# Optimization experiments

Hardware: AMD Instinct MI355X
Metric: run time of the kernel (lower is better)

The kernel has to match this reference:

```python
import jax, jax.numpy as jnp
import numpy as np

HIDDEN = 4096
NUM_HEADS = 32
HEAD_DIM = HIDDEN // NUM_HEADS
B, S = 2, 2048
ROPE_BASE = 10000.0


def setup_inputs() -> dict:
    key = jax.random.key(0)
    k1, k2, k3, k4 = jax.random.split(key, 4)
    hidden_states = jax.random.normal(k1, (B, S, HIDDEN), dtype=jnp.float32)
    positions = jnp.tile(jnp.arange(S, dtype=jnp.int32)[None, :], (B, 1))
    W_qkv = jax.random.normal(k2, (HIDDEN, 3 * HIDDEN), dtype=jnp.float32) * (HIDDEN ** -0.5)
    b_qkv = jax.random.normal(k3, (3 * HIDDEN,), dtype=jnp.float32) * 0.02
    W_o = jax.random.normal(k4, (HIDDEN, HIDDEN), dtype=jnp.float32) * (HIDDEN ** -0.5)
    return {"hidden_states": hidden_states, "positions": positions,
            "W_qkv": W_qkv, "b_qkv": b_qkv, "W_o": W_o}


def _rope(x, positions):
    # x: [B, S, H, D]; GPT-NeoX style full-dim rotary (rotary_dim = head_dim)
    half = HEAD_DIM // 2
    inv_freq = 1.0 / (ROPE_BASE ** (jnp.arange(0, half, dtype=jnp.float32) * 2.0 / HEAD_DIM))
    ang = positions.astype(jnp.float32)[:, :, None] * inv_freq[None, None, :]  # [B,S,half]
    cos = jnp.cos(ang)[:, :, None, :]  # [B,S,1,half]
    sin = jnp.sin(ang)[:, :, None, :]
    x1, x2 = x[..., :half], x[..., half:]
    return jnp.concatenate([x1 * cos - x2 * sin, x2 * cos + x1 * sin], axis=-1)


def reference(hidden_states, positions, W_qkv, b_qkv, W_o):
    qkv = jnp.einsum('bsh,hk->bsk', hidden_states, W_qkv) + b_qkv
    q, k, v = jnp.split(qkv, 3, axis=-1)
    q = q.reshape(B, S, NUM_HEADS, HEAD_DIM)
    k = k.reshape(B, S, NUM_HEADS, HEAD_DIM)
    v = v.reshape(B, S, NUM_HEADS, HEAD_DIM)
    q = _rope(q, positions)
    k = _rope(k, positions)
    scale = HEAD_DIM ** -0.5
    scores = jnp.einsum('bqhd,bkhd->bhqk', q, k) * scale  # [B,H,S,S]
    causal = jnp.tril(jnp.ones((S, S), dtype=bool))
    scores = jnp.where(causal[None, None], scores, jnp.float32(-1e30))
    probs = jax.nn.softmax(scores, axis=-1)
    ctx = jnp.einsum('bhqk,bkhd->bqhd', probs, v).reshape(B, S, HIDDEN)
    return jnp.einsum('bsh,ho->bso', ctx, W_o)
```

## Files before the change

### kernel.cpp

```cpp
#include <hip/hip_runtime.h>
#include <stdint.h>

#define HID 4096
#define NHD 32
#define HD  128
#define BB  2
#define SS  2048
#define BSZ (BB*SS)
#define N3  (3*HID)

typedef __bf16 bf16x8 __attribute__((ext_vector_type(8)));
typedef __bf16 bf16x4 __attribute__((ext_vector_type(4)));
typedef float  f32x4  __attribute__((ext_vector_type(4)));

#define MFMA16(A,B,C) __builtin_amdgcn_mfma_f32_16x16x32_bf16((A),(B),(C),0,0,0)

__device__ __forceinline__ void gl_lds16(const __bf16* g, __bf16* l) {
  __builtin_amdgcn_global_load_lds(
      (__attribute__((address_space(1))) void*)g,
      (__attribute__((address_space(3))) void*)l, 16, 0, 0);
}

__device__ __forceinline__ void block_bar() {
  __builtin_amdgcn_sched_barrier(0);
  __builtin_amdgcn_s_barrier();
  __builtin_amdgcn_sched_barrier(0);
}
#define LGKM0() do { asm volatile("s_waitcnt lgkmcnt(0)" ::: "memory"); \
                     __builtin_amdgcn_sched_barrier(0); } while (0)
#define VMC(n)  do { asm volatile("s_waitcnt vmcnt(" #n ")" ::: "memory"); \
                     __builtin_amdgcn_sched_barrier(0); } while (0)

__global__ void cvt_bf16(const float* __restrict__ in, __bf16* __restrict__ out, int n) {
  int i = (blockIdx.x * blockDim.x + threadIdx.x) * 4;
  if (i >= n) return;
  float4 v = *(const float4*)(in + i);
  bf16x4 r;
  r[0] = (__bf16)v.x; r[1] = (__bf16)v.y; r[2] = (__bf16)v.z; r[3] = (__bf16)v.w;
  *(bf16x4*)(out + i) = r;
}

__global__ void transp_cvt(const float* __restrict__ in, __bf16* __restrict__ out,
                           int R, int C) {
  __shared__ float t[64 * 65];
  int c0 = blockIdx.x * 64, r0 = blockIdx.y * 64;
  int tx = threadIdx.x & 15, ty = threadIdx.x >> 4;
  for (int j = 0; j < 4; ++j) {
    float4 v = *(const float4*)(in + (size_t)(r0 + ty + 16 * j) * C + c0 + tx * 4);
    float* d = t + (ty + 16 * j) * 65 + tx * 4;
    d[0] = v.x; d[1] = v.y; d[2] = v.z; d[3] = v.w;
  }
  __syncthreads();
  for (int j = 0; j < 4; ++j) {
    int cc = ty + 16 * j;
    bf16x4 o4;
    for (int e = 0; e < 4; ++e) o4[e] = (__bf16)t[(tx * 4 + e) * 65 + cc];
    *(bf16x4*)(out + (size_t)(c0 + cc) * R + r0 + tx * 4) = o4;
  }
}


__device__ __forceinline__ void ld_a4(bf16x8 a[4][2], const __bf16* base, int row, int quad) {
#pragma unroll
  for (int m = 0; m < 4; ++m) {
    const int rr = row + m * 16;
    const int sw = rr & 7;
#pragma unroll
    for (int kk = 0; kk < 2; ++kk)
      a[m][kk] = *(const bf16x8*)(base + rr * 64 + ((kk * 4 + quad) ^ sw) * 8);
  }
}
__device__ __forceinline__ void ld_b2(bf16x8 b[2][2], const __bf16* base, int row, int quad) {
#pragma unroll
  for (int n = 0; n < 2; ++n) {
    const int rr = row + n * 16;
    const int sw = rr & 7;
#pragma unroll
    for (int kk = 0; kk < 2; ++kk)
      b[n][kk] = *(const bf16x8*)(base + rr * 64 + ((kk * 4 + quad) ^ sw) * 8);
  }
}
__device__ __forceinline__ void mma_quad(f32x4 acc[8][4], bf16x8 a[4][2],
                                         bf16x8 b[2][2], int mh, int nh) {
  __builtin_amdgcn_s_setprio(1);
#pragma unroll
  for (int m = 0; m < 4; ++m)
#pragma unroll
    for (int n = 0; n < 2; ++n) {
      f32x4 c = acc[mh * 4 + m][nh * 2 + n];
      c = MFMA16(a[m][0], b[n][0], c);
      c = MFMA16(a[m][1], b[n][1], c);
      acc[mh * 4 + m][nh * 2 + n] = c;
    }
  __builtin_amdgcn_s_setprio(0);
}

__device__ __forceinline__ void core256(const __bf16* __restrict__ Ab,
                                        const __bf16* __restrict__ Bb,
                                        int K, __bf16* smem, f32x4 acc[8][4]) {
  const int tid  = threadIdx.x;
  const int wave = tid >> 6, lane = tid & 63;
  const int quad = lane >> 4, l15 = lane & 15;
  const int arow = ((wave >> 2) * 64) + l15;
  const int brow = ((wave & 3) * 32) + l15;
  const int NKT = K >> 6, NIT = NKT >> 1;

  __bf16* aBuf[2] = { smem,          smem + 16384 };
  __bf16* bBuf[2] = { smem + 32768,  smem + 49152 };

  const int off0 = tid * 16, off1 = off0 + 8192;
  const int r0 = off0 >> 7, r1 = off1 >> 7;
  const int sO0 = r0 * K + ((((off0 >> 4) & 7) ^ (r0 & 7)) * 8);
  const int sO1 = r1 * K + ((((off1 >> 4) & 7) ^ (r1 & 7)) * 8);
  const int d0 = off0 >> 1, d1 = off1 >> 1;

#define STG_A(buf, half, kt) do { \
    const __bf16* s_ = Ab + (size_t)(half) * 128 * K + (size_t)(kt) * 64; \
    gl_lds16(s_ + sO0, aBuf[buf] + (half) * 8192 + d0); \
    gl_lds16(s_ + sO1, aBuf[buf] + (half) * 8192 + d1); } while (0)
#define STG_B(buf, half, kt) do { \
    const __bf16* s_ = Bb + (size_t)(half) * 128 * K + (size_t)(kt) * 64; \
    gl_lds16(s_ + sO0, bBuf[buf] + (half) * 8192 + d0); \
    gl_lds16(s_ + sO1, bBuf[buf] + (half) * 8192 + d1); } while (0)

  bf16x8 a_r[4][2], bn0[2][2], bn1[2][2];

  STG_A(0, 0, 0); STG_B(0, 0, 0); STG_B(0, 1, 0); STG_A(0, 1, 0);
  STG_A(1, 0, 1); STG_B(1, 0, 1); STG_B(1, 1, 1);
  VMC(6);
  block_bar();

  for (int i = 0; i < NIT; ++i) {
    const bool last = (i == NIT - 1);
    const int t1 = 2 * i + 1, t2 = 2 * i + 2, t3 = 2 * i + 3;

    ld_a4(a_r, aBuf[0],        arow, quad);
    ld_b2(bn0, bBuf[0],        brow, quad);
    STG_A(1, 1, t1);
    block_bar(); LGKM0();
    mma_quad(acc, a_r, bn0, 0, 0);
    block_bar();

    ld_b2(bn1, bBuf[0] + 8192, brow, quad);
    if (!last) STG_A(0, 0, t2);
    block_bar(); LGKM0();
    mma_quad(acc, a_r, bn1, 0, 1);
    block_bar();

    ld_a4(a_r, aBuf[0] + 8192, arow, quad);
    if (!last) STG_B(0, 0, t2);
    block_bar(); LGKM0();
    mma_quad(acc, a_r, bn1, 1, 1);
    block_bar();

    if (!last) STG_B(0, 1, t2);
    block_bar();
    mma_quad(acc, a_r, bn0, 1, 0);
    if (last) { VMC(0); } else { VMC(6); }
    block_bar();

    ld_a4(a_r, aBuf[1],        arow, quad);
    ld_b2(bn0, bBuf[1],        brow, quad);
    if (!last) STG_A(0, 1, t2);
    block_bar(); LGKM0();
    mma_quad(acc, a_r, bn0, 0, 0);
    block_bar();

    ld_b2(bn1, bBuf[1] + 8192, brow, quad);
    if (!last) STG_A(1, 0, t3);
    block_bar(); LGKM0();
    mma_quad(acc, a_r, bn1, 0, 1);
    block_bar();

    ld_a4(a_r, aBuf[1] + 8192, arow, quad);
    if (!last) STG_B(1, 0, t3);
    block_bar(); LGKM0();
    mma_quad(acc, a_r, bn1, 1, 1);
    block_bar();

    if (!last) STG_B(1, 1, t3);
    block_bar();
    mma_quad(acc, a_r, bn0, 1, 0);
    VMC(6);
    block_bar();
  }
#undef STG_A
#undef STG_B
}

__device__ __forceinline__ int eswz(int r, int c) {
  return r * 256 + ((((c >> 3) ^ (r & 31) ^ (r >> 5)) & 31) * 8) + (c & 7);
}

__global__ __launch_bounds__(512, 2) void gemm_qkv(
    const __bf16* __restrict__ A, const __bf16* __restrict__ Bt,
    const float* __restrict__ bias, const int* __restrict__ pos,
    __bf16* __restrict__ qr, __bf16* __restrict__ kr, __bf16* __restrict__ vt,
    int M, int N, int K) {
  __shared__ __bf16 smem[65536];
  const int tid = threadIdx.x;
  const int wave = tid >> 6, lane = tid & 63;
  const int quad = lane >> 4, l15 = lane & 15;
  const int wm = (wave >> 2) * 64, wn = (wave & 3) * 32;

  const int orig = blockIdx.x;
  const int swz = (orig & 7) * 96 + (orig >> 3);
  const int m0 = (swz & 15) * 256;
  const int n0 = (swz >> 4) * 256;

  f32x4 acc[8][4];
#pragma unroll
  for (int i = 0; i < 8; ++i)
#pragma unroll
    for (int j = 0; j < 4; ++j) acc[i][j] = (f32x4){0.f, 0.f, 0.f, 0.f};

  core256(A + (size_t)m0 * K, Bt + (size_t)n0 * K, K, smem, acc);

#pragma unroll
  for (int ni = 0; ni < 4; ++ni) {
    const int scol = (ni >> 1) * 128 + wn + (ni & 1) * 16 + l15;
    const float bv = bias[n0 + scol];
#pragma unroll
    for (int mi = 0; mi < 8; ++mi) {
      const int rbase = (mi >> 2) * 128 + wm + (mi & 3) * 16 + quad * 4;
#pragma unroll
      for (int rr = 0; rr < 4; ++rr)
        smem[eswz(rbase + rr, scol)] = (__bf16)(acc[mi][ni][rr] + bv);
    }
  }
  __syncthreads();

  const int reg = n0 >> 12;
  const int h0  = (n0 & 4095) >> 7;
  const int b   = m0 >> 11;
  const int s0  = m0 & 2047;

  if (reg == 2) {
    __bf16* dst = vt + (size_t)(b * NHD + h0) * HD * SS;
    const int sg = tid & 31, cb = tid >> 5;
    for (int p = 0; p < 16; ++p) {
      const int c = cb + 16 * p;
      bf16x8 v8;
#pragma unroll
      for (int e = 0; e < 8; ++e) v8[e] = smem[eswz(sg * 8 + e, c)];
      *(bf16x8*)(dst + (size_t)(c >> 7) * HD * SS + (size_t)(c & 127) * SS +
                 s0 + sg * 8) = v8;
    }
  } else {
    __bf16* dst = (reg == 0 ? qr : kr) + (size_t)(b * NHD + h0) * SS * HD;
    const float osc = (reg == 0) ? 0.08838834764831845f : 1.0f;
    const int d2 = tid & 63, rb = (tid >> 6) * 32;
    const float freq = expf(-0.14391156831212787f * (float)d2);
    for (int i = 0; i < 32; ++i) {
      const int r = rb + i;
      const float p = (float)pos[b * SS + s0 + r];
      float sn, cs;
      sincosf(p * freq, &sn, &cs);
#pragma unroll
      for (int hs = 0; hs < 2; ++hs) {
        const float x1 = (float)smem[eswz(r, hs * 128 + d2)];
        const float x2 = (float)smem[eswz(r, hs * 128 + d2 + 64)];
        __bf16* dr = dst + (size_t)hs * SS * HD + (size_t)(s0 + r) * HD;
        dr[d2]      = (__bf16)((x1 * cs - x2 * sn) * osc);
        dr[d2 + 64] = (__bf16)((x2 * cs + x1 * sn) * osc);
      }
    }
  }
}

__global__ __launch_bounds__(512, 2) void gemm_bt(
    const __bf16* __restrict__ A, const __bf16* __restrict__ Bt,
    float* __restrict__ Cout, int M, int N, int K) {
  __shared__ __bf16 smem[65536];
  const int tid = threadIdx.x;
  const int wave = tid >> 6, lane = tid & 63;
  const int quad = lane >> 4, l15 = lane & 15;
  const int wm = (wave >> 2) * 64, wn = (wave & 3) * 32;

  const int orig = blockIdx.x;
  const int swz = (orig & 7) * 32 + (orig >> 3);
  const int m0 = (swz & 15) * 256;
  const int n0 = (swz >> 4) * 256;

  f32x4 acc[8][4];
#pragma unroll
  for (int i = 0; i < 8; ++i)
#pragma unroll
    for (int j = 0; j < 4; ++j) acc[i][j] = (f32x4){0.f, 0.f, 0.f, 0.f};

  core256(A + (size_t)m0 * K, Bt + (size_t)n0 * K, K, smem, acc);

#pragma unroll
  for (int mi = 0; mi < 8; ++mi) {
    const int row = m0 + (mi >> 2) * 128 + wm + (mi & 3) * 16 + quad * 4;
#pragma unroll
    for (int ni = 0; ni < 4; ++ni) {
      const int col = n0 + (ni >> 1) * 128 + wn + (ni & 1) * 16 + l15;
#pragma unroll
      for (int rr = 0; rr < 4; ++rr)
        Cout[(size_t)(row + rr) * N + col] = acc[mi][ni][rr];
    }
  }
}

__global__ __launch_bounds__(256, 2) void flash_attn(
    const __bf16* __restrict__ qr, const __bf16* __restrict__ kr,
    const __bf16* __restrict__ vt, __bf16* __restrict__ ctx) {
  __shared__ __bf16 sK[2][64 * 128];
  __shared__ __bf16 sV[128 * 64];
  __shared__ __bf16 sP[4][32 * 64];
  const int bh = blockIdx.x;
  const int qt = 15 - blockIdx.y;
  const int b = bh >> 5, h = bh & 31;
  const int tid = threadIdx.x;
  const int wave = tid >> 6, lane = tid & 63;
  const int quad = lane >> 4, l15 = lane & 15;
  const int q0 = qt * 128;
  const int NT = 2 * qt + 2;

  const __bf16* qbase = qr + (size_t)bh * SS * HD;
  const __bf16* kbase = kr + (size_t)bh * SS * HD;
  const __bf16* vbase = vt + (size_t)bh * HD * SS;
  __bf16* pw = &sP[wave][0];

#define STG_K(buf_, kt_) do {                                         \
    const __bf16* kb_ = kbase + (size_t)(kt_) * 64 * HD;              \
    _Pragma("unroll")                                                 \
    for (int i_ = 0; i_ < 4; ++i_) {                                  \
      int off_ = tid * 16 + i_ * 4096;                                \
      int r_ = off_ >> 8, cl_ = (off_ >> 4) & 15;                     \
      int cg_ = (cl_ & 8) | ((cl_ & 7) ^ (r_ & 7));                   \
      gl_lds16(kb_ + (size_t)r_ * HD + cg_ * 8, &sK[buf_][0] + (off_ >> 1)); \
    } } while (0)
#define STG_V(kt_) do {                                               \
    const __bf16* vb_ = vbase + (size_t)(kt_) * 64;                   \
    _Pragma("unroll")                                                 \
    for (int i_ = 0; i_ < 4; ++i_) {                                  \
      int off_ = tid * 16 + i_ * 4096;                                \
      int r_ = off_ >> 7, cl_ = (off_ >> 4) & 7;                      \
      int cg_ = cl_ ^ (r_ & 7);                                       \
      gl_lds16(vb_ + (size_t)r_ * SS + cg_ * 8, &sV[0] + (off_ >> 1)); \
    } } while (0)

  bf16x8 qf[2][4];
  for (int im = 0; im < 2; ++im) {
    int row = q0 + wave * 32 + im * 16 + l15;
    for (int ks = 0; ks < 4; ++ks)
      qf[im][ks] = *(const bf16x8*)(qbase + (size_t)row * HD + ks * 32 + quad * 8);
  }

  f32x4 o[2][8];
  for (int im = 0; im < 2; ++im)
    for (int jd = 0; jd < 8; ++jd)
      o[im][jd] = (f32x4){0.f, 0.f, 0.f, 0.f};
  float l_i[2][4];
  for (int im = 0; im < 2; ++im)
    for (int rg = 0; rg < 4; ++rg) l_i[im][rg] = 0.f;

  STG_K(0, 0);

  for (int kt = 0; kt < NT; ++kt) {
    const int k0 = kt * 64;
    const bool more = (kt + 1 < NT);

    block_bar();
    STG_V(kt);
    if (more) STG_K((kt + 1) & 1, kt + 1);
    if (more) { VMC(8); } else { VMC(4); }
    block_bar();

    const __bf16* sKc = &sK[kt & 1][0];

    f32x4 s[2][4];
    for (int im = 0; im < 2; ++im)
      for (int jn = 0; jn < 4; ++jn)
        s[im][jn] = (f32x4){0.f, 0.f, 0.f, 0.f};
    for (int ks = 0; ks < 4; ++ks) {
      bf16x8 kf[4];
      for (int jn = 0; jn < 4; ++jn) {
        int row = jn * 16 + l15;
        int c = ks * 4 + quad;
        int p = (c & 8) | ((c & 7) ^ (row & 7));
        kf[jn] = *(const bf16x8*)(sKc + row * 128 + p * 8);
      }
      for (int im = 0; im < 2; ++im)
        for (int jn = 0; jn < 4; ++jn)
          s[im][jn] = MFMA16(qf[im][ks], kf[jn], s[im][jn]);
    }

    const bool diag = (kt >= 2 * qt);
    for (int im = 0; im < 2; ++im)
      for (int rg = 0; rg < 4; ++rg) {
        int rowg = q0 + wave * 32 + im * 16 + quad * 4 + rg;
        float rs = 0.f;
        for (int jn = 0; jn < 4; ++jn) {
          float p = (diag && (k0 + jn * 16 + l15) > rowg)
                        ? 0.f : __expf(s[im][jn][rg]);
          s[im][jn][rg] = p;
          rs += p;
        }
        for (int d = 1; d < 16; d <<= 1) rs += __shfl_xor(rs, d);
        l_i[im][rg] += rs;
      }

    for (int im = 0; im < 2; ++im)
      for (int jn = 0; jn < 4; ++jn)
        for (int rg = 0; rg < 4; ++rg) {
          int row = im * 16 + quad * 4 + rg;
          int c = jn * 2 + (l15 >> 3);
          pw[row * 64 + ((c ^ (row & 7)) * 8) + (l15 & 7)] =
              (__bf16)s[im][jn][rg];
        }
    LGKM0();
    if (more) { VMC(4); } else { VMC(0); }
    block_bar();

    for (int ks = 0; ks < 2; ++ks) {
      bf16x8 pf[2], vf[8];
      for (int im = 0; im < 2; ++im) {
        int row = im * 16 + l15;
        pf[im] = *(const bf16x8*)(pw + row * 64 +
                                  (((ks * 4 + quad) ^ (row & 7)) * 8));
      }
      for (int jd = 0; jd < 8; ++jd) {
        int row = jd * 16 + l15;
        vf[jd] = *(const bf16x8*)(&sV[0] + row * 64 +
                                  (((ks * 4 + quad) ^ (row & 7)) * 8));
      }
      for (int im = 0; im < 2; ++im)
        for (int jd = 0; jd < 8; ++jd)
          o[im][jd] = MFMA16(pf[im], vf[jd], o[im][jd]);
    }
  }
#undef STG_K
#undef STG_V

  __bf16* cb = ctx + (size_t)(b * SS) * HID + h * HD;
  for (int im = 0; im < 2; ++im)
    for (int rg = 0; rg < 4; ++rg) {
      float inv = 1.0f / l_i[im][rg];
      int row = q0 + wave * 32 + im * 16 + quad * 4 + rg;
      for (int jd = 0; jd < 8; ++jd)
        cb[(size_t)row * HID + jd * 16 + l15] = (__bf16)(o[im][jd][rg] * inv);
    }
}

extern "C" void kernel_launch(void* const* d_in, const int* in_sizes, int n_in,
                              void* d_out, int out_size, void* d_ws, size_t ws_size,
                              hipStream_t stream) {
  const float* hs   = (const float*)d_in[0];
  const int*   pos  = (const int*)d_in[1];
  const float* Wqkv = (const float*)d_in[2];
  const float* bqkv = (const float*)d_in[3];
  const float* Wo   = (const float*)d_in[4];

  char* ws = (char*)d_ws;
  const size_t M32 = 33554432;
  __bf16* hsb   = (__bf16*)(ws);
  __bf16* wqkvT = (__bf16*)(ws + M32);
  __bf16* woT   = (__bf16*)(ws + 4 * M32);
  __bf16* qr    = (__bf16*)(ws + 5 * M32);
  __bf16* kr    = (__bf16*)(ws + 6 * M32);
  __bf16* vt    = (__bf16*)(ws + 7 * M32);
  __bf16* ctx   = hsb;

  cvt_bf16<<<(BSZ * HID) / 1024, 256, 0, stream>>>(hs, hsb, BSZ * HID);
  transp_cvt<<<dim3(N3 / 64, HID / 64), 256, 0, stream>>>(Wqkv, wqkvT, HID, N3);
  transp_cvt<<<dim3(HID / 64, HID / 64), 256, 0, stream>>>(Wo, woT, HID, HID);
  gemm_qkv<<<768, 512, 0, stream>>>(hsb, wqkvT, bqkv, pos, qr, kr, vt,
                                    BSZ, N3, HID);
  flash_attn<<<dim3(BB * NHD, SS / 128), 256, 0, stream>>>(qr, kr, vt, ctx);
  gemm_bt<<<256, 512, 0, stream>>>(ctx, woT, (float*)d_out, BSZ, HID, HID);
}
```

Before: 955.4 us.

## Restructure flash attention: 256-row Q tiles, triple-buffered K/V, MFMA row sums

Flash attention now uses 512-thread blocks that each cover a 256-row query tile, and K and V are loaded together into a three-stage LDS ring. This removes one of the two barriers per key tile and lets loads run two tiles ahead. Block ids are remapped so heads spread across XCDs and causal work is balanced over two passes. Waves skip key tiles that lie entirely above their causal diagonal. The softmax row-sum shuffles are replaced by an extra MFMA of P against a ones vector. The cost is more LDS use (about 128KB per block), which may limit occupancy, and idle waves inside blocks that still span the diagonal.

```diff
diff --git a/kernel.cpp b/kernel.cpp
--- a/kernel.cpp
+++ b/kernel.cpp
@@ -303,143 +303,173 @@
   }
 }
 
-__global__ __launch_bounds__(256, 2) void flash_attn(
+__global__ __launch_bounds__(512, 2) void flash_attn(
     const __bf16* __restrict__ qr, const __bf16* __restrict__ kr,
     const __bf16* __restrict__ vt, __bf16* __restrict__ ctx) {
-  __shared__ __bf16 sK[2][64 * 128];
-  __shared__ __bf16 sV[128 * 64];
-  __shared__ __bf16 sP[4][32 * 64];
-  const int bh = blockIdx.x;
-  const int qt = 15 - blockIdx.y;
+  __shared__ __bf16 sK[3][64 * 128];
+  __shared__ __bf16 sV[3][128 * 64];
+  __shared__ __bf16 sP[8][32 * 64];
+  const int blk  = blockIdx.x;
+  const int slot = blk & 255, pass = blk >> 8;
+  const int xcd  = slot & 7,  jj   = slot >> 3;
+  const int bh   = xcd + 8 * (jj & 7);
+  const int qh   = jj >> 3;
+  const int qt   = pass ? qh : 7 - qh;
   const int b = bh >> 5, h = bh & 31;
   const int tid = threadIdx.x;
   const int wave = tid >> 6, lane = tid & 63;
   const int quad = lane >> 4, l15 = lane & 15;
-  const int q0 = qt * 128;
-  const int NT = 2 * qt + 2;
+  const int q0 = qt * 256;
+  const int NT = 4 * qt + 4;
+  const int wrow = q0 + wave * 32;
+  const int wmax = wrow + 31;
 
   const __bf16* qbase = qr + (size_t)bh * SS * HD;
   const __bf16* kbase = kr + (size_t)bh * SS * HD;
   const __bf16* vbase = vt + (size_t)bh * HD * SS;
   __bf16* pw = &sP[wave][0];
 
-#define STG_K(buf_, kt_) do {                                         \
-    const __bf16* kb_ = kbase + (size_t)(kt_) * 64 * HD;              \
-    _Pragma("unroll")                                                 \
-    for (int i_ = 0; i_ < 4; ++i_) {                                  \
-      int off_ = tid * 16 + i_ * 4096;                                \
-      int r_ = off_ >> 8, cl_ = (off_ >> 4) & 15;                     \
-      int cg_ = (cl_ & 8) | ((cl_ & 7) ^ (r_ & 7));                   \
-      gl_lds16(kb_ + (size_t)r_ * HD + cg_ * 8, &sK[buf_][0] + (off_ >> 1)); \
-    } } while (0)
-#define STG_V(kt_) do {                                               \
-    const __bf16* vb_ = vbase + (size_t)(kt_) * 64;                   \
-    _Pragma("unroll")                                                 \
-    for (int i_ = 0; i_ < 4; ++i_) {                                  \
-      int off_ = tid * 16 + i_ * 4096;                                \
-      int r_ = off_ >> 7, cl_ = (off_ >> 4) & 7;                      \
-      int cg_ = cl_ ^ (r_ & 7);                                       \
-      gl_lds16(vb_ + (size_t)r_ * SS + cg_ * 8, &sV[0] + (off_ >> 1)); \
-    } } while (0)
+  const int offA = tid * 16, offB = offA + 8192;
+  const int krA = offA >> 8, kcA = (offA >> 4) & 15;
+  const int kgA = (kcA & 8) | ((kcA & 7) ^ (krA & 7));
+  const int krB = offB >> 8, kcB = (offB >> 4) & 15;
+  const int kgB = (kcB & 8) | ((kcB & 7) ^ (krB & 7));
+  const int vrA = offA >> 7, vgA = ((offA >> 4) & 7) ^ (vrA & 7);
+  const int vrB = offB >> 7, vgB = ((offB >> 4) & 7) ^ (vrB & 7);
+
+#define STG_KV(buf_, kt_) do {                                            \
+    const __bf16* kb_ = kbase + (size_t)(kt_) * 64 * HD;                  \
+    gl_lds16(kb_ + krA * HD + kgA * 8, &sK[buf_][0] + (offA >> 1));       \
+    gl_lds16(kb_ + krB * HD + kgB * 8, &sK[buf_][0] + (offB >> 1));       \
+    const __bf16* vb_ = vbase + (size_t)(kt_) * 64;                       \
+    gl_lds16(vb_ + (size_t)vrA * SS + vgA * 8, &sV[buf_][0] + (offA >> 1)); \
+    gl_lds16(vb_ + (size_t)vrB * SS + vgB * 8, &sV[buf_][0] + (offB >> 1)); \
+  } while (0)
 
   bf16x8 qf[2][4];
+#pragma unroll
   for (int im = 0; im < 2; ++im) {
-    int row = q0 + wave * 32 + im * 16 + l15;
+    int row = wrow + im * 16 + l15;
+#pragma unroll
     for (int ks = 0; ks < 4; ++ks)
       qf[im][ks] = *(const bf16x8*)(qbase + (size_t)row * HD + ks * 32 + quad * 8);
   }
 
-  f32x4 o[2][8];
-  for (int im = 0; im < 2; ++im)
+  bf16x8 onesf;
+#pragma unroll
+  for (int e = 0; e < 8; ++e) onesf[e] = (__bf16)1.0f;
+
+  f32x4 o[2][8], o_l[2];
+#pragma unroll
+  for (int im = 0; im < 2; ++im) {
+    o_l[im] = (f32x4){0.f, 0.f, 0.f, 0.f};
+#pragma unroll
     for (int jd = 0; jd < 8; ++jd)
       o[im][jd] = (f32x4){0.f, 0.f, 0.f, 0.f};
-  float l_i[2][4];
-  for (int im = 0; im < 2; ++im)
-    for (int rg = 0; rg < 4; ++rg) l_i[im][rg] = 0.f;
-
-  STG_K(0, 0);
+  }
+
+  STG_KV(0, 0); STG_KV(1, 1);
+  int cur = 0;
 
   for (int kt = 0; kt < NT; ++kt) {
     const int k0 = kt * 64;
-    const bool more = (kt + 1 < NT);
-
-    block_bar();
-    STG_V(kt);
-    if (more) STG_K((kt + 1) & 1, kt + 1);
-    if (more) { VMC(8); } else { VMC(4); }
-    block_bar();
-
-    const __bf16* sKc = &sK[kt & 1][0];
-
-    f32x4 s[2][4];
-    for (int im = 0; im < 2; ++im)
-      for (int jn = 0; jn < 4; ++jn)
-        s[im][jn] = (f32x4){0.f, 0.f, 0.f, 0.f};
-    for (int ks = 0; ks < 4; ++ks) {
-      bf16x8 kf[4];
-      for (int jn = 0; jn < 4; ++jn) {
-        int row = jn * 16 + l15;
-        int c = ks * 4 + quad;
-        int p = (c & 8) | ((c & 7) ^ (row & 7));
-        kf[jn] = *(const bf16x8*)(sKc + row * 128 + p * 8);
+    if (kt + 1 < NT) { VMC(4); } else { VMC(0); }
+    block_bar();
+    if (kt + 2 < NT) {
+      int nb = cur + 2; if (nb >= 3) nb -= 3;
+      STG_KV(nb, kt + 2);
+    }
+
+    if (k0 <= wmax) {
+      const __bf16* sKc = &sK[cur][0];
+      const __bf16* sVc = &sV[cur][0];
+
+      f32x4 s[2][4];
+#pragma unroll
+      for (int im = 0; im < 2; ++im)
+#pragma unroll
+        for (int jn = 0; jn < 4; ++jn)
+          s[im][jn] = (f32x4){0.f, 0.f, 0.f, 0.f};
+#pragma unroll
+      for (int ks = 0; ks < 4; ++ks) {
+        bf16x8 kf[4];
+#pragma unroll
+        for (int jn = 0; jn < 4; ++jn) {
+          int row = jn * 16 + l15;
+          int c = ks * 4 + quad;
+          int p = (c & 8) | ((c & 7) ^ (row & 7));
+          kf[jn] = *(const bf16x8*)(sKc + row * 128 + p * 8);
+        }
+#pragma unroll
+        for (int im = 0; im < 2; ++im)
+#pragma unroll
+          for (int jn = 0; jn < 4; ++jn)
+            s[im][jn] = MFMA16(qf[im][ks], kf[jn], s[im][jn]);
       }
+
+      const bool needm = (k0 + 63 > wrow);
+#pragma unroll
       for (int im = 0; im < 2; ++im)
+#pragma unroll
+        for (int rg = 0; rg < 4; ++rg) {
+          int rowg = wrow + im * 16 + quad * 4 + rg;
+#pragma unroll
+          for (int jn = 0; jn < 4; ++jn) {
+            float p = (needm && (k0 + jn * 16 + l15) > rowg)
+                          ? 0.f : __expf(s[im][jn][rg]);
+            s[im][jn][rg] = p;
+          }
+        }
+
+#pragma unroll
+      for (int im = 0; im < 2; ++im)
+#pragma unroll
         for (int jn = 0; jn < 4; ++jn)
-          s[im][jn] = MFMA16(qf[im][ks], kf[jn], s[im][jn]);
-    }
-
-    const bool diag = (kt >= 2 * qt);
-    for (int im = 0; im < 2; ++im)
-      for (int rg = 0; rg < 4; ++rg) {
-        int rowg = q0 + wave * 32 + im * 16 + quad * 4 + rg;
-        float rs = 0.f;
-        for (int jn = 0; jn < 4; ++jn) {
-          float p = (diag && (k0 + jn * 16 + l15) > rowg)
-                        ? 0.f : __expf(s[im][jn][rg]);
-          s[im][jn][rg] = p;
-          rs += p;
+#pragma unroll
+          for (int rg = 0; rg < 4; ++rg) {
+            int row = im * 16 + quad * 4 + rg;
+            int c = jn * 2 + (l15 >> 3);
+            pw[row * 64 + ((c ^ (row & 7)) * 8) + (l15 & 7)] =
+                (__bf16)s[im][jn][rg];
+          }
+      LGKM0();
+
+#pragma unroll
+      for (int ks = 0; ks < 2; ++ks) {
+        bf16x8 pf[2], vf[8];
+#pragma unroll
+        for (int im = 0; im < 2; ++im) {
+          int row = im * 16 + l15;
+          pf[im] = *(const bf16x8*)(pw + row * 64 +
+                                    (((ks * 4 + quad) ^ (row & 7)) * 8));
         }
-        for (int d = 1; d < 16; d <<= 1) rs += __shfl_xor(rs, d);
-        l_i[im][rg] += rs;
+#pragma unroll
+        for (int jd = 0; jd < 8; ++jd) {
+          int row = jd * 16 + l15;
+          vf[jd] = *(const bf16x8*)(sVc + row * 64 +
+                                    (((ks * 4 + quad) ^ (row & 7)) * 8));
+        }
+#pragma unroll
+        for (int im = 0; im < 2; ++im) {
+#pragma unroll
+          for (int jd = 0; jd < 8; ++jd)
+            o[im][jd] = MFMA16(pf[im], vf[jd], o[im][jd]);
+          o_l[im] = MFMA16(pf[im], onesf, o_l[im]);
+        }
       }
-
-    for (int im = 0; im < 2; ++im)
-      for (int jn = 0; jn < 4; ++jn)
-        for (int rg = 0; rg < 4; ++rg) {
-          int row = im * 16 + quad * 4 + rg;
-          int c = jn * 2 + (l15 >> 3);
-          pw[row * 64 + ((c ^ (row & 7)) * 8) + (l15 & 7)] =
-              (__bf16)s[im][jn][rg];
-        }
-    LGKM0();
-    if (more) { VMC(4); } else { VMC(0); }
-    block_bar();
-
-    for (int ks = 0; ks < 2; ++ks) {
-      bf16x8 pf[2], vf[8];
-      for (int im = 0; im < 2; ++im) {
-        int row = im * 16 + l15;
-        pf[im] = *(const bf16x8*)(pw + row * 64 +
-                                  (((ks * 4 + quad) ^ (row & 7)) * 8));
-      }
-      for (int jd = 0; jd < 8; ++jd) {
-        int row = jd * 16 + l15;
-        vf[jd] = *(const bf16x8*)(&sV[0] + row * 64 +
-                                  (((ks * 4 + quad) ^ (row & 7)) * 8));
-      }
-      for (int im = 0; im < 2; ++im)
-        for (int jd = 0; jd < 8; ++jd)
-          o[im][jd] = MFMA16(pf[im], vf[jd], o[im][jd]);
-    }
-  }
-#undef STG_K
-#undef STG_V
+    }
+    cur = (cur + 1 == 3) ? 0 : cur + 1;
+  }
+#undef STG_KV
 
   __bf16* cb = ctx + (size_t)(b * SS) * HID + h * HD;
+#pragma unroll
   for (int im = 0; im < 2; ++im)
+#pragma unroll
     for (int rg = 0; rg < 4; ++rg) {
-      float inv = 1.0f / l_i[im][rg];
-      int row = q0 + wave * 32 + im * 16 + quad * 4 + rg;
+      float inv = 1.0f / o_l[im][rg];
+      int row = wrow + im * 16 + quad * 4 + rg;
+#pragma unroll
       for (int jd = 0; jd < 8; ++jd)
         cb[(size_t)row * HID + jd * 16 + l15] = (__bf16)(o[im][jd][rg] * inv);
     }
@@ -469,6 +499,6 @@
   transp_cvt<<<dim3(HID / 64, HID / 64), 256, 0, stream>>>(Wo, woT, HID, HID);
   gemm_qkv<<<768, 512, 0, stream>>>(hsb, wqkvT, bqkv, pos, qr, kr, vt,
                                     BSZ, N3, HID);
-  flash_attn<<<dim3(BB * NHD, SS / 128), 256, 0, stream>>>(qr, kr, vt, ctx);
+  flash_attn<<<512, 512, 0, stream>>>(qr, kr, vt, ctx);
   gemm_bt<<<256, 512, 0, stream>>>(ctx, woT, (float*)d_out, BSZ, HID, HID);
 }
```

Measured after the change: 954.5 us. No clear change (-0.1%).
